# Performance work log

Hardware: AMD Instinct MI355X
Metric: run time of the kernel (lower is better)

Reference implementation:

```python
import jax, jax.numpy as jnp
import numpy as np

B, S, SIZE = 2048, 512, 96  # size = embedding_size(32) * num_feature(3)


def setup_inputs() -> dict:
    key = jax.random.key(0)
    k1, k2, k3, k4, k5, k6, k7 = jax.random.split(key, 7)
    bound = 1.0 / np.sqrt(SIZE)  # nn.Linear default init range
    return {
        "seq_item_embedding": jax.random.normal(k1, (B, S, SIZE), dtype=jnp.float32),
        "target_item_embedding": jax.random.normal(k2, (B, 1, SIZE), dtype=jnp.float32),
        "mask": jax.random.randint(k3, (B, S + 1, 1), 0, 2).astype(jnp.bool_),
        "w1_weight": jax.random.uniform(k4, (SIZE, SIZE), jnp.float32, -bound, bound),
        "w1_bias": jax.random.uniform(k5, (SIZE,), jnp.float32, -bound, bound),
        "w2_weight": jax.random.uniform(k6, (SIZE, SIZE), jnp.float32, -bound, bound),
        "w2_bias": jax.random.uniform(k7, (SIZE,), jnp.float32, -bound, bound),
    }


def reference(seq_item_embedding, target_item_embedding, mask,
              w1_weight, w1_bias, w2_weight, w2_bias):
    # mask[:, :-1, :] -> [B, S] boolean (True = masked out)
    m = mask[:, :-1, 0]
    # w1(seq): [B, S, size]; note source reassigns seq_item_embedding to this,
    # so the final weighted pool uses the projected sequence.
    seq_h = jnp.einsum('bsd,ed->bse', seq_item_embedding, w1_weight) + w1_bias
    # w2(target): [B, 1, size], broadcasts over seq_len (repeat in torch)
    tgt_h = jnp.einsum('bqd,ed->bqe', target_item_embedding, w2_weight) + w2_bias
    # sigmoid(sum) reduced over feature dim -> scores [B, S]
    scores = jax.nn.sigmoid(seq_h + tgt_h).sum(axis=-1)
    scores = jnp.where(m, jnp.float32(-1e9), scores)
    attn = jax.nn.softmax(scores, axis=-1)  # [B, S]
    # weighted pool over seq dim -> [B, size]
    output = jnp.einsum('bs,bse->be', attn, seq_h)
    return output
```

## Files before the change

### kernel.cpp

```cpp
#include <hip/hip_runtime.h>
#include <math.h>

#define NB 2048
#define NS 512
#define ND 96

typedef __attribute__((ext_vector_type(8))) short short8;
typedef __attribute__((ext_vector_type(4))) float floatx4;

__device__ __forceinline__ unsigned f2bfu(float f) {
    union { float f; unsigned u; } c; c.f = f;
    unsigned u = c.u;
    u += 0x7FFF + ((u >> 16) & 1);
    return u >> 16;
}
__device__ __forceinline__ unsigned pack2(float a, float b) {
    return f2bfu(a) | (f2bfu(b) << 16);
}
__device__ __forceinline__ float lo_f(unsigned u) {
    union { unsigned u; float f; } c; c.u = u << 16; return c.f;
}
__device__ __forceinline__ float hi_f(unsigned u) {
    union { unsigned u; float f; } c; c.u = u & 0xFFFF0000u; return c.f;
}
__device__ __forceinline__ float sigm(float x) {
    return 1.0f / (1.0f + __expf(-x));
}
__device__ __forceinline__ short8 cvt8(floatx4 p0, floatx4 p1) {
    short8 v;
    v[0]=(short)f2bfu(p0[0]); v[1]=(short)f2bfu(p0[1]);
    v[2]=(short)f2bfu(p0[2]); v[3]=(short)f2bfu(p0[3]);
    v[4]=(short)f2bfu(p1[0]); v[5]=(short)f2bfu(p1[1]);
    v[6]=(short)f2bfu(p1[2]); v[7]=(short)f2bfu(p1[3]);
    return v;
}

__global__ __launch_bounds__(512, 3)
void attn_fused(const float* __restrict__ seq,
                const float* __restrict__ tgt,
                const int*   __restrict__ mask,
                const float* __restrict__ w1,
                const float* __restrict__ b1,
                const float* __restrict__ w2,
                const float* __restrict__ b2,
                float* __restrict__ out)
{
    __shared__ short w1f[18 * 64 * 8];
    __shared__ floatx4 thp4[ND];
    __shared__ float red2[8];
    __shared__ float osum[8][ND];

    const int b    = blockIdx.x;
    const int tid  = threadIdx.x;
    const int lane = tid & 63;
    const int wave = tid >> 6;
    const int l15  = lane & 15;
    const int quad = lane >> 4;

    const int m = mask[(size_t)b * (NS + 1) + tid];

    for (int idx = tid; idx < 1152; idx += 512) {
        const int e  = idx / 12;
        const int dc = idx - 12 * e;
        const int kk = dc >> 2;
        const int q  = dc & 3;
        const float* p = w1 + e * ND + kk * 32 + q * 8;
        floatx4 p0 = *(const floatx4*)(p);
        floatx4 p1 = *(const floatx4*)(p + 4);
        const int t = e >> 4, r = e & 15;
        *(short8*)&w1f[(((t * 3 + kk) * 64) + q * 16 + r) * 8] = cvt8(p0, p1);
    }

    if (tid < 4 * ND) {
        const int e    = tid >> 2;
        const int part = tid & 3;
        const float* tv = tgt + (size_t)b * ND + part * 24;
        const float* wr = w2 + e * ND + part * 24;
        float acc = 0.f;
        #pragma unroll
        for (int d = 0; d < 24; d += 4) {
            floatx4 a = *(const floatx4*)(tv + d);
            floatx4 w = *(const floatx4*)(wr + d);
            acc += a[0]*w[0] + a[1]*w[1] + a[2]*w[2] + a[3]*w[3];
        }
        thp4[e][part] = acc;
    }
    __syncthreads();

    float tgtv[6], biasv[6];
    #pragma unroll
    for (int t = 0; t < 6; ++t) {
        const int e = 16 * t + l15;
        floatx4 tp = thp4[e];
        tgtv[t]  = b2[e] + tp[0] + tp[1] + tp[2] + tp[3];
        biasv[t] = b1[e];
    }

    const float* abase = seq + ((size_t)b * NS + l15) * ND + quad * 8;
    unsigned pk[4][6][2];
    float myscore = 0.f;

    #pragma unroll
    for (int sti = 0; sti < 4; ++sti) {
        const int s0 = (wave * 4 + sti) * 16;
        short8 af[3];
        #pragma unroll
        for (int kk = 0; kk < 3; ++kk) {
            const float* p = abase + (size_t)s0 * ND + kk * 32;
            af[kk] = cvt8(*(const floatx4*)(p), *(const floatx4*)(p + 4));
        }
        float p0s = 0.f, p1s = 0.f, p2s = 0.f, p3s = 0.f;
        #pragma unroll
        for (int t = 0; t < 6; ++t) {
            floatx4 acc = { biasv[t], biasv[t], biasv[t], biasv[t] };
            #pragma unroll
            for (int kk = 0; kk < 3; ++kk) {
                const short8 bf = *(const short8*)&w1f[((t * 3 + kk) * 64 + lane) * 8];
                acc = __builtin_amdgcn_mfma_f32_16x16x32_bf16(af[kk], bf, acc, 0, 0, 0);
            }
            pk[sti][t][0] = pack2(acc[0], acc[1]);
            pk[sti][t][1] = pack2(acc[2], acc[3]);
            const float thv = tgtv[t];
            p0s += sigm(acc[0] + thv);
            p1s += sigm(acc[1] + thv);
            p2s += sigm(acc[2] + thv);
            p3s += sigm(acc[3] + thv);
        }
        #pragma unroll
        for (int off = 1; off < 16; off <<= 1) {
            p0s += __shfl_xor(p0s, off, 64);
            p1s += __shfl_xor(p1s, off, 64);
            p2s += __shfl_xor(p2s, off, 64);
            p3s += __shfl_xor(p3s, off, 64);
        }
        float pv = p0s;
        pv = ((lane & 3) == 1) ? p1s : pv;
        pv = ((lane & 3) == 2) ? p2s : pv;
        pv = ((lane & 3) == 3) ? p3s : pv;
        const int src = (((lane >> 2) & 3) << 4) | (lane & 3);
        const float g = __shfl(pv, src, 64);
        if ((lane >> 4) == sti) myscore = g;
    }

    float e0 = (m != 0) ? 0.0f : __expf(myscore - 96.0f);
    float ssum = e0;
    #pragma unroll
    for (int off = 1; off < 64; off <<= 1) ssum += __shfl_xor(ssum, off, 64);
    if (lane == 0) red2[wave] = ssum;
    __syncthreads();
    float tot = red2[0];
    #pragma unroll
    for (int w = 1; w < 8; ++w) tot += red2[w];
    const float atv = e0 * (1.0f / tot);

    float o[6] = {0.f, 0.f, 0.f, 0.f, 0.f, 0.f};
    #pragma unroll
    for (int sti = 0; sti < 4; ++sti) {
        const int sb = sti * 16 + quad * 4;
        const float a0 = __shfl(atv, sb + 0, 64);
        const float a1 = __shfl(atv, sb + 1, 64);
        const float a2 = __shfl(atv, sb + 2, 64);
        const float a3 = __shfl(atv, sb + 3, 64);
        #pragma unroll
        for (int t = 0; t < 6; ++t) {
            const unsigned u0 = pk[sti][t][0];
            const unsigned u1 = pk[sti][t][1];
            o[t] += a0 * lo_f(u0) + a1 * hi_f(u0) + a2 * lo_f(u1) + a3 * hi_f(u1);
        }
    }
    #pragma unroll
    for (int t = 0; t < 6; ++t) {
        o[t] += __shfl_xor(o[t], 16, 64);
        o[t] += __shfl_xor(o[t], 32, 64);
    }
    if (quad == 0) {
        #pragma unroll
        for (int t = 0; t < 6; ++t) osum[wave][16 * t + l15] = o[t];
    }
    __syncthreads();
    if (tid < ND) {
        float a = 0.f;
        #pragma unroll
        for (int w = 0; w < 8; ++w) a += osum[w][tid];
        out[(size_t)b * ND + tid] = a;
    }
}

extern "C" void kernel_launch(void* const* d_in, const int* in_sizes, int n_in,
                              void* d_out, int out_size, void* d_ws, size_t ws_size,
                              hipStream_t stream) {
    const float* seq  = (const float*)d_in[0];
    const float* tgt  = (const float*)d_in[1];
    const int*   mask = (const int*)d_in[2];
    const float* w1   = (const float*)d_in[3];
    const float* b1   = (const float*)d_in[4];
    const float* w2   = (const float*)d_in[5];
    const float* b2   = (const float*)d_in[6];
    float* out = (float*)d_out;
    attn_fused<<<dim3(NB), dim3(512), 0, stream>>>(seq, tgt, mask, w1, b1, w2, b2, out);
}
```

Measured before the change: 670.0 us.

## Fuse softmax-weighted pooling into score loop with fixed-shift exponent

Instead of keeping packed bf16 projections for all 64 rows per thread and pooling after the softmax reduction, each 16-row tile's exp-weights are computed immediately (fixed shift of 48, mask staged as floats in shared memory). The tile's fp32 projections are accumulated into the output right away, and normalization is deferred to the final store. This removes the pk register array and the shuffle-based score redistribution, which lowers register pressure and allows launch bounds to be raised to 4 blocks per SM. The fixed shift relies on scores being bounded in [0,96], and weighting now uses fp32 rather than bf16-rounded projections.

```diff
diff --git a/kernel.cpp b/kernel.cpp
--- a/kernel.cpp
+++ b/kernel.cpp
@@ -14,15 +14,6 @@
     u += 0x7FFF + ((u >> 16) & 1);
     return u >> 16;
 }
-__device__ __forceinline__ unsigned pack2(float a, float b) {
-    return f2bfu(a) | (f2bfu(b) << 16);
-}
-__device__ __forceinline__ float lo_f(unsigned u) {
-    union { unsigned u; float f; } c; c.u = u << 16; return c.f;
-}
-__device__ __forceinline__ float hi_f(unsigned u) {
-    union { unsigned u; float f; } c; c.u = u & 0xFFFF0000u; return c.f;
-}
 __device__ __forceinline__ float sigm(float x) {
     return 1.0f / (1.0f + __expf(-x));
 }
@@ -35,7 +26,7 @@
     return v;
 }
 
-__global__ __launch_bounds__(512, 3)
+__global__ __launch_bounds__(512, 4)
 void attn_fused(const float* __restrict__ seq,
                 const float* __restrict__ tgt,
                 const int*   __restrict__ mask,
@@ -47,6 +38,7 @@
 {
     __shared__ short w1f[18 * 64 * 8];
     __shared__ floatx4 thp4[ND];
+    __shared__ float maskf[NS];
     __shared__ float red2[8];
     __shared__ float osum[8][ND];
 
@@ -57,7 +49,7 @@
     const int l15  = lane & 15;
     const int quad = lane >> 4;
 
-    const int m = mask[(size_t)b * (NS + 1) + tid];
+    maskf[tid] = (mask[(size_t)b * (NS + 1) + tid] != 0) ? 0.0f : 1.0f;
 
     for (int idx = tid; idx < 1152; idx += 512) {
         const int e  = idx / 12;
@@ -97,8 +89,8 @@
     }
 
     const float* abase = seq + ((size_t)b * NS + l15) * ND + quad * 8;
-    unsigned pk[4][6][2];
-    float myscore = 0.f;
+    float o_acc[6] = {0.f, 0.f, 0.f, 0.f, 0.f, 0.f};
+    float sacc = 0.f;
 
     #pragma unroll
     for (int sti = 0; sti < 4; ++sti) {
@@ -109,6 +101,7 @@
             const float* p = abase + (size_t)s0 * ND + kk * 32;
             af[kk] = cvt8(*(const floatx4*)(p), *(const floatx4*)(p + 4));
         }
+        floatx4 acc6[6];
         float p0s = 0.f, p1s = 0.f, p2s = 0.f, p3s = 0.f;
         #pragma unroll
         for (int t = 0; t < 6; ++t) {
@@ -118,8 +111,7 @@
                 const short8 bf = *(const short8*)&w1f[((t * 3 + kk) * 64 + lane) * 8];
                 acc = __builtin_amdgcn_mfma_f32_16x16x32_bf16(af[kk], bf, acc, 0, 0, 0);
             }
-            pk[sti][t][0] = pack2(acc[0], acc[1]);
-            pk[sti][t][1] = pack2(acc[2], acc[3]);
+            acc6[t] = acc;
             const float thv = tgtv[t];
             p0s += sigm(acc[0] + thv);
             p1s += sigm(acc[1] + thv);
@@ -133,56 +125,43 @@
             p2s += __shfl_xor(p2s, off, 64);
             p3s += __shfl_xor(p3s, off, 64);
         }
-        float pv = p0s;
-        pv = ((lane & 3) == 1) ? p1s : pv;
-        pv = ((lane & 3) == 2) ? p2s : pv;
-        pv = ((lane & 3) == 3) ? p3s : pv;
-        const int src = (((lane >> 2) & 3) << 4) | (lane & 3);
-        const float g = __shfl(pv, src, 64);
-        if ((lane >> 4) == sti) myscore = g;
+        const int sq = s0 + quad * 4;
+        const float e0 = maskf[sq + 0] * __expf(p0s - 48.f);
+        const float e1 = maskf[sq + 1] * __expf(p1s - 48.f);
+        const float e2 = maskf[sq + 2] * __expf(p2s - 48.f);
+        const float e3 = maskf[sq + 3] * __expf(p3s - 48.f);
+        sacc += e0 + e1 + e2 + e3;
+        #pragma unroll
+        for (int t = 0; t < 6; ++t) {
+            o_acc[t] += e0 * acc6[t][0] + e1 * acc6[t][1]
+                      + e2 * acc6[t][2] + e3 * acc6[t][3];
+        }
     }
 
-    float e0 = (m != 0) ? 0.0f : __expf(myscore - 96.0f);
-    float ssum = e0;
-    #pragma unroll
-    for (int off = 1; off < 64; off <<= 1) ssum += __shfl_xor(ssum, off, 64);
-    if (lane == 0) red2[wave] = ssum;
+    float ss = sacc;
+    ss += __shfl_xor(ss, 16, 64);
+    ss += __shfl_xor(ss, 32, 64);
+    if (lane == 0) red2[wave] = ss;
     __syncthreads();
     float tot = red2[0];
     #pragma unroll
     for (int w = 1; w < 8; ++w) tot += red2[w];
-    const float atv = e0 * (1.0f / tot);
 
-    float o[6] = {0.f, 0.f, 0.f, 0.f, 0.f, 0.f};
-    #pragma unroll
-    for (int sti = 0; sti < 4; ++sti) {
-        const int sb = sti * 16 + quad * 4;
-        const float a0 = __shfl(atv, sb + 0, 64);
-        const float a1 = __shfl(atv, sb + 1, 64);
-        const float a2 = __shfl(atv, sb + 2, 64);
-        const float a3 = __shfl(atv, sb + 3, 64);
-        #pragma unroll
-        for (int t = 0; t < 6; ++t) {
-            const unsigned u0 = pk[sti][t][0];
-            const unsigned u1 = pk[sti][t][1];
-            o[t] += a0 * lo_f(u0) + a1 * hi_f(u0) + a2 * lo_f(u1) + a3 * hi_f(u1);
-        }
-    }
     #pragma unroll
     for (int t = 0; t < 6; ++t) {
-        o[t] += __shfl_xor(o[t], 16, 64);
-        o[t] += __shfl_xor(o[t], 32, 64);
+        o_acc[t] += __shfl_xor(o_acc[t], 16, 64);
+        o_acc[t] += __shfl_xor(o_acc[t], 32, 64);
     }
     if (quad == 0) {
         #pragma unroll
-        for (int t = 0; t < 6; ++t) osum[wave][16 * t + l15] = o[t];
+        for (int t = 0; t < 6; ++t) osum[wave][16 * t + l15] = o_acc[t];
     }
     __syncthreads();
     if (tid < ND) {
         float a = 0.f;
         #pragma unroll
         for (int w = 0; w < 8; ++w) a += osum[w][tid];
-        out[(size_t)b * ND + tid] = a;
+        out[(size_t)b * ND + tid] = a * (1.0f / tot);
     }
 }
 
```

Measured after the change: 733.4 us. +9.5%, slower.
